# Kernel tuning notes

Measured on AMD Instinct MI355X. Metric: run time of the kernel, lower is better.

## Reference

```python
import jax, jax.numpy as jnp
import numpy as np

B, T, S, D, H, E, K, FF = 4, 1024, 1024, 1024, 16, 8, 2, 4096
DH = D // H
EPS = 1e-5

def layernorm(x, g, b):
    m = x.mean(-1, keepdims=True)
    v = x.var(-1, keepdims=True)
    return (x - m) / jnp.sqrt(v + EPS) * g + b

def mha(q, k, v, mask, wq, bq, wk, bk, wv, bv, wo, bo):
    Bq, Tq, _ = q.shape
    Tk = k.shape[1]
    Q = (q @ wq + bq).reshape(Bq, Tq, H, DH).transpose(0, 2, 1, 3)
    Kh = (k @ wk + bk).reshape(Bq, Tk, H, DH).transpose(0, 2, 1, 3)
    V = (v @ wv + bv).reshape(Bq, Tk, H, DH).transpose(0, 2, 1, 3)
    scores = jnp.einsum('bhqd,bhkd->bhqk', Q, Kh) / (DH ** 0.5)
    scores = jnp.where(mask != 0, scores, jnp.float32(-1e9))
    A = jax.nn.softmax(scores, axis=-1)
    O = jnp.einsum('bhqk,bhkd->bhqd', A, V).transpose(0, 2, 1, 3).reshape(Bq, Tq, D)
    return O @ wo + bo

def sparse_moe(x, wg, bg, w1, b1, w2, b2):
    # x: [B,T,D] -> tokens [N,D]
    Bx, Tx, _ = x.shape
    xt = x.reshape(-1, D)
    N = xt.shape[0]
    probs = jax.nn.softmax(xt @ wg + bg, axis=-1)          # [N,E]
    topv, topi = jax.lax.top_k(probs, K)                    # [N,K]
    topv = topv / topv.sum(-1, keepdims=True)
    gates = jnp.zeros((N, E), xt.dtype).at[jnp.arange(N)[:, None], topi].set(topv)
    h = jax.nn.relu(jnp.einsum('nd,edh->enh', xt, w1) + b1[:, None, :])  # [E,N,FF]
    y = jnp.einsum('enh,ehd->end', h, w2) + b2[:, None, :]               # [E,N,D]
    out = jnp.einsum('ne,end->nd', gates, y)
    return out.reshape(Bx, Tx, D)

def setup_inputs() -> dict:
    key = jax.random.key(0)
    ks = jax.random.split(key, 32)
    r = lambda k, s: jax.random.normal(k, s, dtype=jnp.float32) * 0.02
    inp = {
        'x': jax.random.normal(ks[0], (B, T, D), jnp.float32),
        'encoder_out': jax.random.normal(ks[1], (B, S, D), jnp.float32),
        'src_attn_mask': jnp.ones((B, 1, 1, S), jnp.int32),
        'tgt_attn_mask': jnp.tril(jnp.ones((T, T), jnp.int32))[None, None],
        'ln1_g': jnp.ones((D,), jnp.float32), 'ln1_b': jnp.zeros((D,), jnp.float32),
        'ln2_g': jnp.ones((D,), jnp.float32), 'ln2_b': jnp.zeros((D,), jnp.float32),
        'ln3_g': jnp.ones((D,), jnp.float32), 'ln3_b': jnp.zeros((D,), jnp.float32),
        'wq1': r(ks[2], (D, D)), 'bq1': jnp.zeros((D,), jnp.float32),
        'wk1': r(ks[3], (D, D)), 'bk1': jnp.zeros((D,), jnp.float32),
        'wv1': r(ks[4], (D, D)), 'bv1': jnp.zeros((D,), jnp.float32),
        'wo1': r(ks[5], (D, D)), 'bo1': jnp.zeros((D,), jnp.float32),
        'wq2': r(ks[6], (D, D)), 'bq2': jnp.zeros((D,), jnp.float32),
        'wk2': r(ks[7], (D, D)), 'bk2': jnp.zeros((D,), jnp.float32),
        'wv2': r(ks[8], (D, D)), 'bv2': jnp.zeros((D,), jnp.float32),
        'wo2': r(ks[9], (D, D)), 'bo2': jnp.zeros((D,), jnp.float32),
        'wg': r(ks[10], (D, E)), 'bg': jnp.zeros((E,), jnp.float32),
        'w1': r(ks[11], (E, D, FF)), 'b1': jnp.zeros((E, FF), jnp.float32),
        'w2': r(ks[12], (E, FF, D)), 'b2': jnp.zeros((E, D), jnp.float32),
    }
    return inp

def reference(x, encoder_out, src_attn_mask, tgt_attn_mask,
              ln1_g, ln1_b, ln2_g, ln2_b, ln3_g, ln3_b,
              wq1, bq1, wk1, bk1, wv1, bv1, wo1, bo1,
              wq2, bq2, wk2, bk2, wv2, bv2, wo2, bo2,
              wg, bg, w1, b1, w2, b2):
    # pre-norm residual: x + sublayer(LN(x)); dropout=0 (eval)
    n1 = layernorm(x, ln1_g, ln1_b)
    h1 = x + mha(n1, n1, n1, tgt_attn_mask, wq1, bq1, wk1, bk1, wv1, bv1, wo1, bo1)
    n2 = layernorm(h1, ln2_g, ln2_b)
    h2 = h1 + mha(n2, encoder_out, encoder_out, src_attn_mask, wq2, bq2, wk2, bk2, wv2, bv2, wo2, bo2)
    n3 = layernorm(h2, ln3_g, ln3_b)
    h3 = h2 + sparse_moe(n3, wg, bg, w1, b1, w2, b2)
    return h3
```

## Files before the change

kernel.cpp:

```cpp
#include <hip/hip_runtime.h>

typedef unsigned short u16;
typedef float f32x4 __attribute__((ext_vector_type(4)));
typedef short s16x8 __attribute__((ext_vector_type(8)));
typedef u16   u16x4 __attribute__((ext_vector_type(4)));

#define DEV static __device__ __forceinline__

DEV u16 f2b(float f){
  unsigned u = __builtin_bit_cast(unsigned, f);
  u += 0x7fffu + ((u >> 16) & 1u);
  return (u16)(u >> 16);
}
DEV float b2f(u16 h){ unsigned u = ((unsigned)h) << 16; return __builtin_bit_cast(float, u); }
DEV void tsplit(float v, u16& hv, u16& lv){
  unsigned u = __builtin_bit_cast(unsigned, v);
  hv = (u16)(u >> 16);
  float rest = v - __builtin_bit_cast(float, u & 0xffff0000u);
  lv = (u16)(__builtin_bit_cast(unsigned, rest) >> 16);
}
DEV float fexp2(float x){ float r; asm("v_exp_f32 %0, %1" : "=v"(r) : "v"(x)); return r; }

DEV void glds16(const u16* g, u16* l){
  __builtin_amdgcn_global_load_lds(
      (const __attribute__((address_space(1))) void*)g,
      (__attribute__((address_space(3))) void*)l, 16, 0, 0);
}

DEV f32x4 mfma3(s16x8 ah, s16x8 al, s16x8 bh, s16x8 bl, f32x4 c){
  c = __builtin_amdgcn_mfma_f32_16x16x32_bf16(ah, bh, c, 0, 0, 0);
  c = __builtin_amdgcn_mfma_f32_16x16x32_bf16(ah, bl, c, 0, 0, 0);
  c = __builtin_amdgcn_mfma_f32_16x16x32_bf16(al, bh, c, 0, 0, 0);
  return c;
}

constexpr int TT = 1024, DM = 1024, NE = 8, FFD = 4096;
constexpr int NTOK = 4096;

struct Ptr8 { const float* p[8]; };

__global__ __launch_bounds__(256) void trans8_k(Ptr8 srcs, u16* __restrict__ dh, u16* __restrict__ dl){
  __shared__ float tl[64][65];
  const float* src = srcs.p[blockIdx.z];
  u16* dsth = dh + (size_t)blockIdx.z * 1024 * 1024;
  u16* dstl = dl + (size_t)blockIdx.z * 1024 * 1024;
  const int tid = threadIdx.x;
  const int r0 = blockIdx.y * 64, c0 = blockIdx.x * 64;
  const int ty = tid >> 4, tx = tid & 15;
#pragma unroll
  for (int i = 0; i < 4; i++){
    int row = ty + i * 16;
    f32x4 v = *(const f32x4*)&src[(size_t)(r0 + row) * 1024 + c0 + tx * 4];
#pragma unroll
    for (int j = 0; j < 4; j++) tl[row][tx * 4 + j] = v[j];
  }
  __syncthreads();
#pragma unroll
  for (int i = 0; i < 4; i++){
    int drow = ty + i * 16;
    u16x4 oh, ol;
#pragma unroll
    for (int j = 0; j < 4; j++){
      float v = tl[tx * 4 + j][drow];
      u16 hh, ll; tsplit(v, hh, ll);
      oh[j] = hh; ol[j] = ll;
    }
    *(u16x4*)&dsth[(size_t)(c0 + drow) * 1024 + r0 + tx * 4] = oh;
    *(u16x4*)&dstl[(size_t)(c0 + drow) * 1024 + r0 + tx * 4] = ol;
  }
}

__global__ __launch_bounds__(256) void transb_k(const float* __restrict__ src0, u16* __restrict__ dst0, int R, int C){
  __shared__ float tl[64][65];
  const float* src = src0 + (size_t)blockIdx.z * R * C;
  u16* dst = dst0 + (size_t)blockIdx.z * R * C;
  const int tid = threadIdx.x;
  const int r0 = blockIdx.y * 64, c0 = blockIdx.x * 64;
  const int ty = tid >> 4, tx = tid & 15;
#pragma unroll
  for (int i = 0; i < 4; i++){
    int row = ty + i * 16;
    f32x4 v = *(const f32x4*)&src[(size_t)(r0 + row) * C + c0 + tx * 4];
#pragma unroll
    for (int j = 0; j < 4; j++) tl[row][tx * 4 + j] = v[j];
  }
  __syncthreads();
#pragma unroll
  for (int i = 0; i < 4; i++){
    int drow = ty + i * 16;
    u16x4 o;
#pragma unroll
    for (int j = 0; j < 4; j++) o[j] = f2b(tl[tx * 4 + j][drow]);
    *(u16x4*)&dst[(size_t)(c0 + drow) * R + r0 + tx * 4] = o;
  }
}

__global__ __launch_bounds__(256) void split_k(const float* __restrict__ src,
                                               u16* __restrict__ dh, u16* __restrict__ dl, int n4){
  int i = blockIdx.x * 256 + threadIdx.x;
  if (i < n4){
    f32x4 v = *(const f32x4*)&src[(size_t)i * 4];
    u16x4 oh, ol;
#pragma unroll
    for (int j = 0; j < 4; j++){ u16 hh, ll; tsplit(v[j], hh, ll); oh[j] = hh; ol[j] = ll; }
    *(u16x4*)&dh[(size_t)i * 4] = oh;
    *(u16x4*)&dl[(size_t)i * 4] = ol;
  }
}

__global__ __launch_bounds__(256) void ln_k(const float* __restrict__ x, const float* __restrict__ g,
                                            const float* __restrict__ b,
                                            u16* __restrict__ outH, u16* __restrict__ outL){
  __shared__ float red[8];
  const int row = blockIdx.x, tid = threadIdx.x, l = tid & 63, wave = tid >> 6;
  f32x4 v = *(const f32x4*)&x[(size_t)row * DM + tid * 4];
  float s = v[0] + v[1] + v[2] + v[3];
  float sq = v[0]*v[0] + v[1]*v[1] + v[2]*v[2] + v[3]*v[3];
#pragma unroll
  for (int m = 1; m < 64; m <<= 1){ s += __shfl_xor(s, m); sq += __shfl_xor(sq, m); }
  if (l == 0){ red[wave] = s; red[4 + wave] = sq; }
  __syncthreads();
  float tot = red[0] + red[1] + red[2] + red[3];
  float totq = red[4] + red[5] + red[6] + red[7];
  float mean = tot * (1.0f / DM);
  float var = totq * (1.0f / DM) - mean * mean;
  float rstd = rsqrtf(var + 1e-5f);
  f32x4 gg = *(const f32x4*)&g[tid * 4];
  f32x4 bb = *(const f32x4*)&b[tid * 4];
  u16x4 oh, ol;
#pragma unroll
  for (int j = 0; j < 4; j++){
    float y = (v[j] - mean) * rstd * gg[j] + bb[j];
    u16 hh, ll; tsplit(y, hh, ll); oh[j] = hh; ol[j] = ll;
  }
  *(u16x4*)&outH[(size_t)row * DM + tid * 4] = oh;
  if (outL) *(u16x4*)&outL[(size_t)row * DM + tid * 4] = ol;
}

struct QKVArgs {
  const u16* ah[3]; const u16* al[3]; const float* bias[3];
};

__global__ __launch_bounds__(256) void gemm_qkv3_k(
    QKVArgs args, const u16* __restrict__ Bhp, const u16* __restrict__ Blp,
    u16* __restrict__ QH, u16* __restrict__ QL,
    u16* __restrict__ KH, u16* __restrict__ KL,
    u16* __restrict__ VTH, u16* __restrict__ VTL)
{
  constexpr int K = DM;
  __shared__ alignas(16) u16 LAh[128 * 32], LAl[128 * 32];
  __shared__ alignas(16) u16 LBh[64 * 32], LBl[64 * 32];
  const int tid = threadIdx.x, l = tid & 63, wave = tid >> 6;
  const int seg = blockIdx.z;
  const int m0 = blockIdx.y * 128, n0 = blockIdx.x * 64;
  const int r0 = tid >> 2, seg8 = (tid & 3) * 8;
  const u16* gAh = args.ah[seg] + (size_t)(m0 + r0) * K + seg8;
  const u16* gAl = args.al[seg] + (size_t)(m0 + r0) * K + seg8;
  const u16* gBh = Bhp + (size_t)(seg * 1024 + n0 + r0) * K + seg8;
  const u16* gBl = Blp + (size_t)(seg * 1024 + n0 + r0) * K + seg8;
  u16* wAh = &LAh[wave * 512]; u16* wAl = &LAl[wave * 512];
  u16* wBh = &LBh[wave * 512]; u16* wBl = &LBl[wave * 512];
  const size_t K64 = (size_t)64 * K;
  f32x4 acc[4][2];
#pragma unroll
  for (int i = 0; i < 4; i++)
#pragma unroll
    for (int j = 0; j < 2; j++) acc[i][j] = f32x4{0.f, 0.f, 0.f, 0.f};
  const int wm = (wave >> 1) * 64, wn = (wave & 1) * 32;
  for (int kt = 0; kt < K; kt += 32){
    __syncthreads();
    glds16(gAh + kt, wAh); glds16(gAh + kt + K64, wAh + 2048);
    glds16(gAl + kt, wAl); glds16(gAl + kt + K64, wAl + 2048);
    glds16(gBh + kt, wBh);
    glds16(gBl + kt, wBl);
    __syncthreads();
    s16x8 afh[4], afl[4], bfh[2], bfl[2];
#pragma unroll
    for (int i = 0; i < 4; i++){
      int ar = (wm + i * 16 + (l & 15)) * 32 + (l >> 4) * 8;
      afh[i] = *(const s16x8*)&LAh[ar];
      afl[i] = *(const s16x8*)&LAl[ar];
    }
#pragma unroll
    for (int j = 0; j < 2; j++){
      int br = (wn + j * 16 + (l & 15)) * 32 + (l >> 4) * 8;
      bfh[j] = *(const s16x8*)&LBh[br];
      bfl[j] = *(const s16x8*)&LBl[br];
    }
#pragma unroll
    for (int i = 0; i < 4; i++)
#pragma unroll
      for (int j = 0; j < 2; j++)
        acc[i][j] = mfma3(afh[i], afl[i], bfh[j], bfl[j], acc[i][j]);
  }
  const float* bp = args.bias[seg];
  u16* DH = (seg == 0) ? QH : KH;
  u16* DL = (seg == 0) ? QL : KL;
#pragma unroll
  for (int i = 0; i < 4; i++)
#pragma unroll
    for (int r = 0; r < 4; r++){
      int row = m0 + wm + i * 16 + (l >> 4) * 4 + r;
#pragma unroll
      for (int j = 0; j < 2; j++){
        int col = n0 + wn + j * 16 + (l & 15);
        float v = acc[i][j][r] + bp[col];
        u16 hv, lv; tsplit(v, hv, lv);
        if (seg == 2){
          int bb = row >> 10, tq = row & 1023, hh = col >> 6, dd = col & 63;
          size_t vi = ((size_t)((bb << 4) + hh) * 64 + dd) * 1024 + tq;
          VTH[vi] = hv; VTL[vi] = lv;
        } else {
          size_t idx = (size_t)row * 1024 + col;
          DH[idx] = hv; DL[idx] = lv;
        }
      }
    }
}

__global__ __launch_bounds__(256) void gemm_o64_k(
    const u16* __restrict__ Ahp, const u16* __restrict__ Alp,
    const u16* __restrict__ Bhp, const u16* __restrict__ Blp,
    const float* __restrict__ bias, const float* __restrict__ res,
    float* __restrict__ Cf)
{
  constexpr int K = DM;
  __shared__ alignas(16) u16 LAh[64 * 32], LAl[64 * 32];
  __shared__ alignas(16) u16 LBh[64 * 32], LBl[64 * 32];
  const int tid = threadIdx.x, l = tid & 63, wave = tid >> 6;
  const int m0 = blockIdx.y * 64, n0 = blockIdx.x * 64;
  const int rA = tid >> 2, seg8 = (tid & 3) * 8;
  const u16* gAh = Ahp + (size_t)(m0 + rA) * K + seg8;
  const u16* gAl = Alp + (size_t)(m0 + rA) * K + seg8;
  const u16* gBh = Bhp + (size_t)(n0 + rA) * K + seg8;
  const u16* gBl = Blp + (size_t)(n0 + rA) * K + seg8;
  u16* wAh = &LAh[wave * 512]; u16* wAl = &LAl[wave * 512];
  u16* wBh = &LBh[wave * 512]; u16* wBl = &LBl[wave * 512];
  f32x4 acc[2][2];
#pragma unroll
  for (int i = 0; i < 2; i++)
#pragma unroll
    for (int j = 0; j < 2; j++) acc[i][j] = f32x4{0.f, 0.f, 0.f, 0.f};
  const int wm = (wave >> 1) * 32, wn = (wave & 1) * 32;
  for (int kt = 0; kt < K; kt += 32){
    __syncthreads();
    glds16(gAh + kt, wAh);
    glds16(gAl + kt, wAl);
    glds16(gBh + kt, wBh);
    glds16(gBl + kt, wBl);
    __syncthreads();
    s16x8 afh[2], afl[2], bfh[2], bfl[2];
#pragma unroll
    for (int i = 0; i < 2; i++){
      int ar = (wm + i * 16 + (l & 15)) * 32 + (l >> 4) * 8;
      afh[i] = *(const s16x8*)&LAh[ar];
      afl[i] = *(const s16x8*)&LAl[ar];
    }
#pragma unroll
    for (int j = 0; j < 2; j++){
      int br = (wn + j * 16 + (l & 15)) * 32 + (l >> 4) * 8;
      bfh[j] = *(const s16x8*)&LBh[br];
      bfl[j] = *(const s16x8*)&LBl[br];
    }
#pragma unroll
    for (int i = 0; i < 2; i++)
#pragma unroll
      for (int j = 0; j < 2; j++)
        acc[i][j] = mfma3(afh[i], afl[i], bfh[j], bfl[j], acc[i][j]);
  }
#pragma unroll
  for (int i = 0; i < 2; i++)
#pragma unroll
    for (int r = 0; r < 4; r++){
      int row = m0 + wm + i * 16 + (l >> 4) * 4 + r;
#pragma unroll
      for (int j = 0; j < 2; j++){
        int col = n0 + wn + j * 16 + (l & 15);
        size_t idx = (size_t)row * 1024 + col;
        Cf[idx] = acc[i][j][r] + bias[col] + res[idx];
      }
    }
}

template<bool CAUSAL>
__global__ __launch_bounds__(512) void attn5_k(
    const u16* __restrict__ Qh, const u16* __restrict__ Ql,
    const u16* __restrict__ Kh, const u16* __restrict__ Kl,
    const u16* __restrict__ Vth, const u16* __restrict__ Vtl,
    const int* __restrict__ mask,
    float* __restrict__ OP0, float* __restrict__ OP1,
    float* __restrict__ LS0, float* __restrict__ LS1,
    int Tq, int Tk)
{
  constexpr float CS = 0.125f * 1.4426950408889634f;
  __shared__ alignas(16) u16 KhiL[2048], KloL[2048];
  __shared__ alignas(16) u16 VhiL[2048], VloL[2048];
  __shared__ alignas(16) u16 Plh[8][640], Pll[8][640];
  const int tid = threadIdx.x, l = tid & 63, wave = tid >> 6;
  const int id = blockIdx.x;
  const int bh = ((id >> 3) & 7) * 8 + (id & 7);
  const int b = bh >> 4, h = bh & 15;
  const int qt = (id >> 6) & 7, ks = id >> 9;
  const int q0 = qt * 128;
  float* __restrict__ OP = ks ? OP1 : OP0;
  float* __restrict__ LS = ks ? LS1 : LS0;
  const int ktBeg = ks * 512;
  int lim = CAUSAL ? (q0 + 128) : Tk;
  if (lim > Tk) lim = Tk;
  int ktEnd = (ks + 1) * 512;
  if (ktEnd > lim) ktEnd = lim;

  const int qr = q0 + wave * 16 + (l & 15);
  s16x8 qah[2], qal[2];
#pragma unroll
  for (int kb = 0; kb < 2; kb++){
    size_t base = (size_t)(b * Tq + qr) * DM + h * 64 + kb * 32 + (l >> 4) * 8;
    qah[kb] = *(const s16x8*)(Qh + base);
    qal[kb] = *(const s16x8*)(Ql + base);
  }

  const int sHalf = wave >> 2;
  const int sw = wave & 3;
  const int iS = sw * 64 + l;
  const int keyS = iS >> 3, cKS = iS & 7;
  const u16* gK = (sHalf ? Kl : Kh)
      + (size_t)(b * Tk + ktBeg + keyS) * DM + h * 64 + ((cKS ^ (keyS & 7)) * 8);
  u16* dK = (sHalf ? KloL : KhiL) + sw * 512;
  const int dS = iS >> 2, cVS = iS & 3;
  const size_t vgbase = (size_t)bh * 64 * 1024;
  const u16* gV = (sHalf ? Vtl : Vth)
      + vgbase + (size_t)dS * 1024 + ktBeg + ((cVS ^ ((dS >> 1) & 3)) * 8);
  u16* dV = (sHalf ? VloL : VhiL) + sw * 512;

  float lsum[4] = {0.f, 0.f, 0.f, 0.f};
  f32x4 oacc[4];
#pragma unroll
  for (int nb = 0; nb < 4; nb++) oacc[nb] = f32x4{0.f, 0.f, 0.f, 0.f};
  const int qgr = q0 + wave * 16 + (l >> 4) * 4;

  for (int kt = ktBeg; kt < ktEnd; kt += 32){
    __syncthreads();
    glds16(gK, dK); gK += (size_t)32 * DM;
    glds16(gV, dV); gV += 32;
    __syncthreads();

    f32x4 s[2];
#pragma unroll
    for (int n = 0; n < 2; n++){
      s[n] = f32x4{0.f, 0.f, 0.f, 0.f};
      const int key = n * 16 + (l & 15);
      const int sK = (key & 7);
#pragma unroll
      for (int kb = 0; kb < 2; kb++){
        const int cK = kb * 4 + (l >> 4);
        const int off = key * 64 + ((cK ^ sK) * 8);
        s16x8 kh = *(const s16x8*)&KhiL[off];
        s16x8 klo = *(const s16x8*)&KloL[off];
        s[n] = __builtin_amdgcn_mfma_f32_16x16x32_bf16(qah[kb], kh, s[n], 0, 0, 0);
        s[n] = __builtin_amdgcn_mfma_f32_16x16x32_bf16(qah[kb], klo, s[n], 0, 0, 0);
        s[n] = __builtin_amdgcn_mfma_f32_16x16x32_bf16(qal[kb], kh, s[n], 0, 0, 0);
      }
    }
    int key0 = kt + (l & 15), key1 = key0 + 16;
    int mv0 = 1, mv1 = 1;
    if (!CAUSAL && mask){ mv0 = mask[b * Tk + key0]; mv1 = mask[b * Tk + key1]; }
#pragma unroll
    for (int r = 0; r < 4; r++){
      float p0, p1;
      if (CAUSAL){
        int qg = qgr + r;
        p0 = (key0 <= qg) ? fexp2(s[0][r] * CS) : 0.f;
        p1 = (key1 <= qg) ? fexp2(s[1][r] * CS) : 0.f;
      } else {
        p0 = mv0 ? fexp2(s[0][r] * CS) : 0.f;
        p1 = mv1 ? fexp2(s[1][r] * CS) : 0.f;
      }
      lsum[r] += p0 + p1;
      int po = ((l >> 4) * 4 + r) * 40 + (l & 15);
      u16 h0, l0, h1, l1;
      tsplit(p0, h0, l0); tsplit(p1, h1, l1);
      Plh[wave][po] = h0;      Pll[wave][po] = l0;
      Plh[wave][po + 16] = h1; Pll[wave][po + 16] = l1;
    }
    s16x8 pah = *(const s16x8*)&Plh[wave][(l & 15) * 40 + (l >> 4) * 8];
    s16x8 pal = *(const s16x8*)&Pll[wave][(l & 15) * 40 + (l >> 4) * 8];
#pragma unroll
    for (int nb = 0; nb < 4; nb++){
      const int d = nb * 16 + (l & 15);
      const int off = d * 32 + (((l >> 4) ^ ((d >> 1) & 3)) * 8);
      s16x8 vfh = *(const s16x8*)&VhiL[off];
      s16x8 vfl = *(const s16x8*)&VloL[off];
      oacc[nb] = mfma3(pah, pal, vfh, vfl, oacc[nb]);
    }
  }
#pragma unroll
  for (int r = 0; r < 4; r++){
    float s = lsum[r];
    s += __shfl_xor(s, 1); s += __shfl_xor(s, 2);
    s += __shfl_xor(s, 4); s += __shfl_xor(s, 8);
    int qg = qgr + r;
    if ((l & 15) == 0) LS[(size_t)bh * 1024 + qg] = s;
#pragma unroll
    for (int nb = 0; nb < 4; nb++)
      OP[(size_t)(b * Tq + qg) * DM + h * 64 + nb * 16 + (l & 15)] = oacc[nb][r];
  }
}

__global__ __launch_bounds__(256) void norm_k(
    const float* __restrict__ OP0, const float* __restrict__ OP1,
    const float* __restrict__ LS0, const float* __restrict__ LS1,
    u16* __restrict__ Oh, u16* __restrict__ Ol)
{
  const int t = blockIdx.x, c = threadIdx.x * 4;
  const int b = t >> 10, q = t & 1023, h = c >> 6;
  const size_t li = (size_t)(b * 16 + h) * 1024 + q;
  float inv = 1.0f / (LS0[li] + LS1[li]);
  f32x4 o0 = *(const f32x4*)&OP0[(size_t)t * DM + c];
  f32x4 o1 = *(const f32x4*)&OP1[(size_t)t * DM + c];
  u16x4 oh, ol;
#pragma unroll
  for (int j = 0; j < 4; j++){
    float v = (o0[j] + o1[j]) * inv;
    u16 hh, ll; tsplit(v, hh, ll); oh[j] = hh; ol[j] = ll;
  }
  *(u16x4*)&Oh[(size_t)t * DM + c] = oh;
  *(u16x4*)&Ol[(size_t)t * DM + c] = ol;
}

__global__ __launch_bounds__(256) void moe_gate_k(const float* __restrict__ X,
    const float* __restrict__ g3, const float* __restrict__ b3,
    const float* __restrict__ wg, const float* __restrict__ bg,
    int* __restrict__ cnt, int* __restrict__ perm,
    int* __restrict__ toke, int* __restrict__ tokp, float* __restrict__ tokg)
{
  const int wave = threadIdx.x >> 6, l = threadIdx.x & 63;
  const int t = blockIdx.x * 4 + wave;
  float xv[16];
  float s = 0.f, sq = 0.f;
#pragma unroll
  for (int i = 0; i < 16; i++){
    xv[i] = X[(size_t)t * DM + l + i * 64];
    s += xv[i]; sq += xv[i] * xv[i];
  }
#pragma unroll
  for (int m = 1; m < 64; m <<= 1){ s += __shfl_xor(s, m); sq += __shfl_xor(sq, m); }
  float mean = s * (1.0f / DM);
  float var = sq * (1.0f / DM) - mean * mean;
  float rstd = rsqrtf(var + 1e-5f);
  float acc[8];
#pragma unroll
  for (int e = 0; e < 8; e++) acc[e] = 0.f;
#pragma unroll
  for (int i = 0; i < 16; i++){
    int k = l + i * 64;
    float xn = (xv[i] - mean) * rstd * g3[k] + b3[k];
    f32x4 wa = *(const f32x4*)&wg[k * 8];
    f32x4 wb = *(const f32x4*)&wg[k * 8 + 4];
#pragma unroll
    for (int j = 0; j < 4; j++){ acc[j] += xn * wa[j]; acc[4 + j] += xn * wb[j]; }
  }
#pragma unroll
  for (int e = 0; e < 8; e++)
#pragma unroll
    for (int m = 1; m < 64; m <<= 1) acc[e] += __shfl_xor(acc[e], m);
  if (l == 0){
    float lg[8];
#pragma unroll
    for (int e = 0; e < 8; e++) lg[e] = acc[e] + bg[e];
    float mx = lg[0];
#pragma unroll
    for (int e = 1; e < 8; e++) mx = fmaxf(mx, lg[e]);
    float ex[8]; float sum = 0.f;
#pragma unroll
    for (int e = 0; e < 8; e++){ ex[e] = expf(lg[e] - mx); sum += ex[e]; }
    int i0 = 0;
    for (int e = 1; e < 8; e++) if (ex[e] > ex[i0]) i0 = e;
    int i1 = (i0 == 0) ? 1 : 0;
    for (int e = 0; e < 8; e++) if (e != i0 && ex[e] > ex[i1]) i1 = e;
    float p0 = ex[i0] / sum, p1 = ex[i1] / sum;
    float gs = p0 + p1;
    int pos0 = atomicAdd(&cnt[i0], 1);
    int pos1 = atomicAdd(&cnt[i1], 1);
    perm[i0 * 4096 + pos0] = t;
    perm[i1 * 4096 + pos1] = t;
    toke[2 * t] = i0; toke[2 * t + 1] = i1;
    tokp[2 * t] = pos0; tokp[2 * t + 1] = pos1;
    tokg[2 * t] = p0 / gs; tokg[2 * t + 1] = p1 / gs;
  }
}

__global__ void offsets_k(const int* __restrict__ cnt, int* __restrict__ off){
  if (threadIdx.x == 0){
    int a = 0;
    for (int e = 0; e < 8; e++){ off[e] = a; a += cnt[e]; }
  }
}

__global__ __launch_bounds__(256) void gemm_moe1_k(
    const u16* __restrict__ X, const u16* __restrict__ W1t, const float* __restrict__ b1,
    const int* __restrict__ perm, const int* __restrict__ cnt, const int* __restrict__ off,
    u16* __restrict__ Hb)
{
  const int e = blockIdx.z;
  const int Ce = cnt[e];
  const int mt = blockIdx.y;
  if (mt * 128 >= Ce) return;
  __shared__ alignas(16) u16 Asl[2][128 * 32];
  __shared__ alignas(16) u16 Bsl[2][64 * 32];
  const int tid = threadIdx.x, l = tid & 63, wave = tid >> 6;
  const int n0 = blockIdx.x * 64;
  const int r0 = tid >> 2, seg = (tid & 3) * 8;
  const int rl0 = mt * 128 + r0, rl1 = rl0 + 64;
  const int g0 = perm[e * 4096 + (rl0 < Ce ? rl0 : Ce - 1)];
  const int g1 = perm[e * 4096 + (rl1 < Ce ? rl1 : Ce - 1)];
  const u16* gA0 = X + (size_t)g0 * DM + seg;
  const u16* gA1 = X + (size_t)g1 * DM + seg;
  const u16* gB = W1t + (size_t)e * FFD * DM + (size_t)(n0 + r0) * DM + seg;
  u16* wA0 = &Asl[0][wave * 512]; u16* wA1 = &Asl[1][wave * 512];
  u16* wB0 = &Bsl[0][wave * 512]; u16* wB1 = &Bsl[1][wave * 512];
  f32x4 acc[4][2];
#pragma unroll
  for (int i = 0; i < 4; i++)
#pragma unroll
    for (int j = 0; j < 2; j++) acc[i][j] = f32x4{0.f,0.f,0.f,0.f};
  const int wm = (wave >> 1) * 64, wn = (wave & 1) * 32;
  for (int kt = 0; kt < DM; kt += 64){
    __syncthreads();
    glds16(gA0 + kt, wA0);      glds16(gA1 + kt, wA0 + 2048);
    glds16(gA0 + kt + 32, wA1); glds16(gA1 + kt + 32, wA1 + 2048);
    glds16(gB + kt, wB0);
    glds16(gB + kt + 32, wB1);
    __syncthreads();
#pragma unroll
    for (int p = 0; p < 2; p++){
      s16x8 af[4], bfr[2];
#pragma unroll
      for (int i = 0; i < 4; i++)
        af[i]  = *(const s16x8*)&Asl[p][(wm + i * 16 + (l & 15)) * 32 + (l >> 4) * 8];
#pragma unroll
      for (int j = 0; j < 2; j++)
        bfr[j] = *(const s16x8*)&Bsl[p][(wn + j * 16 + (l & 15)) * 32 + (l >> 4) * 8];
#pragma unroll
      for (int i = 0; i < 4; i++)
#pragma unroll
        for (int j = 0; j < 2; j++)
          acc[i][j] = __builtin_amdgcn_mfma_f32_16x16x32_bf16(af[i], bfr[j], acc[i][j], 0, 0, 0);
    }
  }
  const int base = off[e];
#pragma unroll
  for (int i = 0; i < 4; i++)
#pragma unroll
    for (int r = 0; r < 4; r++){
      int rloc = mt * 128 + wm + i * 16 + (l >> 4) * 4 + r;
      if (rloc < Ce){
#pragma unroll
        for (int j = 0; j < 2; j++){
          int col = n0 + wn + j * 16 + (l & 15);
          float v = acc[i][j][r] + b1[e * FFD + col];
          v = fmaxf(v, 0.f);
          Hb[(size_t)(base + rloc) * FFD + col] = f2b(v);
        }
      }
    }
}

__global__ __launch_bounds__(256) void gemm_moe2_k(
    const u16* __restrict__ Hb, const u16* __restrict__ W2t,
    const int* __restrict__ cnt, const int* __restrict__ off,
    u16* __restrict__ YP0, u16* __restrict__ YP1)
{
  const int z = blockIdx.z;
  const int e = z & 7, ks = z >> 3;
  const int Ce = cnt[e];
  const int mt = blockIdx.y;
  if (mt * 128 >= Ce) return;
  u16* __restrict__ Y = ks ? YP1 : YP0;
  __shared__ alignas(16) u16 Asl[2][128 * 32];
  __shared__ alignas(16) u16 Bsl[2][64 * 32];
  const int tid = threadIdx.x, l = tid & 63, wave = tid >> 6;
  const int n0 = blockIdx.x * 64;
  const int r0 = tid >> 2, seg = (tid & 3) * 8;
  const int base = off[e];
  const int rl0 = mt * 128 + r0, rl1 = rl0 + 64;
  const int a0r = base + (rl0 < Ce ? rl0 : Ce - 1);
  const int a1r = base + (rl1 < Ce ? rl1 : Ce - 1);
  const u16* gA0 = Hb + (size_t)a0r * FFD + seg;
  const u16* gA1 = Hb + (size_t)a1r * FFD + seg;
  const u16* gB = W2t + (size_t)e * DM * FFD + (size_t)(n0 + r0) * FFD + seg;
  u16* wA0 = &Asl[0][wave * 512]; u16* wA1 = &Asl[1][wave * 512];
  u16* wB0 = &Bsl[0][wave * 512]; u16* wB1 = &Bsl[1][wave * 512];
  f32x4 acc[4][2];
#pragma unroll
  for (int i = 0; i < 4; i++)
#pragma unroll
    for (int j = 0; j < 2; j++) acc[i][j] = f32x4{0.f,0.f,0.f,0.f};
  const int wm = (wave >> 1) * 64, wn = (wave & 1) * 32;
  const int kBeg = ks * (FFD / 2), kEnd = kBeg + FFD / 2;
  for (int kt = kBeg; kt < kEnd; kt += 64){
    __syncthreads();
    glds16(gA0 + kt, wA0);      glds16(gA1 + kt, wA0 + 2048);
    glds16(gA0 + kt + 32, wA1); glds16(gA1 + kt + 32, wA1 + 2048);
    glds16(gB + kt, wB0);
    glds16(gB + kt + 32, wB1);
    __syncthreads();
#pragma unroll
    for (int p = 0; p < 2; p++){
      s16x8 af[4], bfr[2];
#pragma unroll
      for (int i = 0; i < 4; i++)
        af[i]  = *(const s16x8*)&Asl[p][(wm + i * 16 + (l & 15)) * 32 + (l >> 4) * 8];
#pragma unroll
      for (int j = 0; j < 2; j++)
        bfr[j] = *(const s16x8*)&Bsl[p][(wn + j * 16 + (l & 15)) * 32 + (l >> 4) * 8];
#pragma unroll
      for (int i = 0; i < 4; i++)
#pragma unroll
        for (int j = 0; j < 2; j++)
          acc[i][j] = __builtin_amdgcn_mfma_f32_16x16x32_bf16(af[i], bfr[j], acc[i][j], 0, 0, 0);
    }
  }
#pragma unroll
  for (int i = 0; i < 4; i++)
#pragma unroll
    for (int r = 0; r < 4; r++){
      int rloc = mt * 128 + wm + i * 16 + (l >> 4) * 4 + r;
      if (rloc < Ce){
#pragma unroll
        for (int j = 0; j < 2; j++){
          int col = n0 + wn + j * 16 + (l & 15);
          Y[(size_t)(base + rloc) * DM + col] = f2b(acc[i][j][r]);
        }
      }
    }
}

__global__ __launch_bounds__(256) void combine_k(const float* __restrict__ h2,
    const u16* __restrict__ YP0, const u16* __restrict__ YP1,
    const int* __restrict__ toke, const int* __restrict__ tokp, const float* __restrict__ tokg,
    const int* __restrict__ off, const float* __restrict__ b2, float* __restrict__ out)
{
  const int t = blockIdx.x;
  const int c = threadIdx.x * 4;
  int e0 = toke[2 * t], e1 = toke[2 * t + 1];
  size_t r0 = (size_t)off[e0] + tokp[2 * t];
  size_t r1 = (size_t)off[e1] + tokp[2 * t + 1];
  float g0 = tokg[2 * t], g1 = tokg[2 * t + 1];
  f32x4 a  = *(const f32x4*)&h2[(size_t)t * DM + c];
  u16x4 ya0 = *(const u16x4*)&YP0[r0 * DM + c];
  u16x4 ya1 = *(const u16x4*)&YP1[r0 * DM + c];
  u16x4 yb0 = *(const u16x4*)&YP0[r1 * DM + c];
  u16x4 yb1 = *(const u16x4*)&YP1[r1 * DM + c];
  f32x4 v0 = *(const f32x4*)&b2[(size_t)e0 * DM + c];
  f32x4 v1 = *(const f32x4*)&b2[(size_t)e1 * DM + c];
  f32x4 o;
#pragma unroll
  for (int j = 0; j < 4; j++){
    float yA = b2f(ya0[j]) + b2f(ya1[j]);
    float yB = b2f(yb0[j]) + b2f(yb1[j]);
    o[j] = a[j] + (yA + v0[j]) * g0 + (yB + v1[j]) * g1;
  }
  *(f32x4*)&out[(size_t)t * DM + c] = o;
}

extern "C" void kernel_launch(void* const* d_in, const int* in_sizes, int n_in,
                              void* d_out, int out_size, void* d_ws, size_t ws_size,
                              hipStream_t stream) {
  const float* x    = (const float*)d_in[0];
  const float* enc  = (const float*)d_in[1];
  const int* smask  = (const int*)d_in[2];
  const float* ln1g = (const float*)d_in[4]; const float* ln1b = (const float*)d_in[5];
  const float* ln2g = (const float*)d_in[6]; const float* ln2b = (const float*)d_in[7];
  const float* ln3g = (const float*)d_in[8]; const float* ln3b = (const float*)d_in[9];
  const float* wq1 = (const float*)d_in[10]; const float* bq1 = (const float*)d_in[11];
  const float* wk1 = (const float*)d_in[12]; const float* bk1 = (const float*)d_in[13];
  const float* wv1 = (const float*)d_in[14]; const float* bv1 = (const float*)d_in[15];
  const float* wo1 = (const float*)d_in[16]; const float* bo1 = (const float*)d_in[17];
  const float* wq2 = (const float*)d_in[18]; const float* bq2 = (const float*)d_in[19];
  const float* wk2 = (const float*)d_in[20]; const float* bk2 = (const float*)d_in[21];
  const float* wv2 = (const float*)d_in[22]; const float* bv2 = (const float*)d_in[23];
  const float* wo2 = (const float*)d_in[24]; const float* bo2 = (const float*)d_in[25];
  const float* wg  = (const float*)d_in[26]; const float* bg  = (const float*)d_in[27];
  const float* w1  = (const float*)d_in[28]; const float* b1  = (const float*)d_in[29];
  const float* w2  = (const float*)d_in[30]; const float* b2  = (const float*)d_in[31];

  const size_t MB = 1024ull * 1024ull;
  char* ws = (char*)d_ws;
  size_t o = 0;
  auto alloc = [&](size_t bytes) -> void* {
    void* p = ws + o;
    o += (bytes + 255) & ~(size_t)255;
    return p;
  };
  float* H1  = (float*)alloc(16 * MB);
  float* H2  = (float*)alloc(16 * MB);
  u16*  NBF  = (u16*) alloc(8 * MB);
  int* CNT  = (int*)alloc(256);
  int* OFF  = (int*)alloc(256);
  int* PERM = (int*)alloc((size_t)8 * 4096 * 4);
  int* TOKE = (int*)alloc((size_t)NTOK * 2 * 4);
  int* TOKP = (int*)alloc((size_t)NTOK * 2 * 4);
  float* TOKG = (float*)alloc((size_t)NTOK * 2 * 4);
  char* R = (char*)alloc(224 * MB);
  u16* WTH = (u16*)(R);
  u16* WTL = (u16*)(R + 16 * MB);
  u16* NH  = (u16*)(R + 32 * MB);
  u16* NL  = (u16*)(R + 40 * MB);
  u16* EH  = (u16*)(R + 48 * MB);
  u16* EL  = (u16*)(R + 56 * MB);
  u16* QH  = (u16*)(R + 64 * MB);
  u16* QL  = (u16*)(R + 72 * MB);
  u16* KH  = (u16*)(R + 80 * MB);
  u16* KL  = (u16*)(R + 88 * MB);
  u16* VTH = (u16*)(R + 96 * MB);
  u16* VTL = (u16*)(R + 104 * MB);
  u16* OH  = (u16*)(R + 112 * MB);
  u16* OL  = (u16*)(R + 120 * MB);
  float* OP0 = (float*)(R + 128 * MB);
  float* OP1 = (float*)(R + 144 * MB);
  float* LS0 = (float*)(R + 160 * MB);
  float* LS1 = (float*)(R + 161 * MB);
  u16* W1T = (u16*)(R);
  u16* W2T = (u16*)(R + 64 * MB);
  u16* HB  = (u16*)(R + 128 * MB);
  u16* YP0 = (u16*)(R + 192 * MB);
  u16* YP1 = (u16*)(R + 208 * MB);

  Ptr8 p8; p8.p[0]=wq1; p8.p[1]=wk1; p8.p[2]=wv1; p8.p[3]=wo1;
           p8.p[4]=wq2; p8.p[5]=wk2; p8.p[6]=wv2; p8.p[7]=wo2;
  trans8_k<<<dim3(16,16,8), 256, 0, stream>>>(p8, WTH, WTL);
  split_k<<<dim3(4096), 256, 0, stream>>>(enc, EH, EL, NTOK * DM / 4);

  const size_t W = (size_t)1024 * 1024;
  ln_k<<<dim3(NTOK), 256, 0, stream>>>(x, ln1g, ln1b, NH, NL);
  {
    QKVArgs a;
    a.ah[0]=NH; a.ah[1]=NH; a.ah[2]=NH;
    a.al[0]=NL; a.al[1]=NL; a.al[2]=NL;
    a.bias[0]=bq1; a.bias[1]=bk1; a.bias[2]=bv1;
    gemm_qkv3_k<<<dim3(16,32,3), 256, 0, stream>>>(a, WTH + 0*W, WTL + 0*W,
                                                   QH, QL, KH, KL, VTH, VTL);
  }
  attn5_k<true><<<dim3(1024), 512, 0, stream>>>(QH, QL, KH, KL, VTH, VTL, nullptr,
                                                OP0, OP1, LS0, LS1, TT, TT);
  norm_k<<<dim3(NTOK), 256, 0, stream>>>(OP0, OP1, LS0, LS1, OH, OL);
  gemm_o64_k<<<dim3(16,64), 256, 0, stream>>>(OH, OL, WTH + 3*W, WTL + 3*W, bo1, x, H1);

  ln_k<<<dim3(NTOK), 256, 0, stream>>>(H1, ln2g, ln2b, NH, NL);
  {
    QKVArgs a;
    a.ah[0]=NH; a.ah[1]=EH; a.ah[2]=EH;
    a.al[0]=NL; a.al[1]=EL; a.al[2]=EL;
    a.bias[0]=bq2; a.bias[1]=bk2; a.bias[2]=bv2;
    gemm_qkv3_k<<<dim3(16,32,3), 256, 0, stream>>>(a, WTH + 4*W, WTL + 4*W,
                                                   QH, QL, KH, KL, VTH, VTL);
  }
  attn5_k<false><<<dim3(1024), 512, 0, stream>>>(QH, QL, KH, KL, VTH, VTL, smask,
                                                 OP0, OP1, LS0, LS1, TT, TT);
  norm_k<<<dim3(NTOK), 256, 0, stream>>>(OP0, OP1, LS0, LS1, OH, OL);
  gemm_o64_k<<<dim3(16,64), 256, 0, stream>>>(OH, OL, WTH + 7*W, WTL + 7*W, bo2, H1, H2);

  transb_k<<<dim3(64,16,8), 256, 0, stream>>>(w1, W1T, 1024, 4096);
  transb_k<<<dim3(16,64,8), 256, 0, stream>>>(w2, W2T, 4096, 1024);
  ln_k<<<dim3(NTOK), 256, 0, stream>>>(H2, ln3g, ln3b, NBF, nullptr);
  hipMemsetAsync(CNT, 0, 8 * sizeof(int), stream);
  moe_gate_k<<<dim3(1024), 256, 0, stream>>>(H2, ln3g, ln3b, wg, bg, CNT, PERM, TOKE, TOKP, TOKG);
  offsets_k<<<dim3(1), 64, 0, stream>>>(CNT, OFF);
  gemm_moe1_k<<<dim3(64,32,8), 256, 0, stream>>>(NBF, W1T, b1, PERM, CNT, OFF, HB);
  gemm_moe2_k<<<dim3(16,32,16), 256, 0, stream>>>(HB, W2T, CNT, OFF, YP0, YP1);
  combine_k<<<dim3(NTOK), 256, 0, stream>>>(H2, YP0, YP1, TOKE, TOKP, TOKG, OFF, b2, (float*)d_out);
}
```

Baseline: 900.2 us.

## Enlarge MoE down-projection tile to 128x128, drop split-K, emit fp32 output

The second expert GEMM now uses 512-thread blocks computing 128x128 output tiles over the full FF dimension, instead of 128x64 tiles split in two along K. Blocks are indexed through a flattened 1D grid with the expert in the low bits. The result is written once in fp32, and the combine kernel reads a single fp32 buffer instead of summing two bf16 partials. The aim is more operand reuse per loaded tile and no partial-sum traffic. In exchange there are fewer and longer blocks, which may worsen load balance and tail effects, and fp32 stores double the bytes per output element.

```diff
diff --git a/kernel.cpp b/kernel.cpp
--- a/kernel.cpp
+++ b/kernel.cpp
@@ -565,28 +565,25 @@
     }
 }
 
-__global__ __launch_bounds__(256) void gemm_moe2_k(
+__global__ __launch_bounds__(512) void gemm_moe2_k(
     const u16* __restrict__ Hb, const u16* __restrict__ W2t,
-    const int* __restrict__ cnt, const int* __restrict__ off,
-    u16* __restrict__ YP0, u16* __restrict__ YP1)
+    const int* __restrict__ cnt, const int* __restrict__ off, float* __restrict__ Y)
 {
-  const int z = blockIdx.z;
-  const int e = z & 7, ks = z >> 3;
+  const int id = blockIdx.x;
+  const int e = id & 7;
+  const int rest = id >> 3;
+  const int n0 = (rest & 7) * 128;
+  const int mt = rest >> 3;
   const int Ce = cnt[e];
-  const int mt = blockIdx.y;
   if (mt * 128 >= Ce) return;
-  u16* __restrict__ Y = ks ? YP1 : YP0;
   __shared__ alignas(16) u16 Asl[2][128 * 32];
-  __shared__ alignas(16) u16 Bsl[2][64 * 32];
+  __shared__ alignas(16) u16 Bsl[2][128 * 32];
   const int tid = threadIdx.x, l = tid & 63, wave = tid >> 6;
-  const int n0 = blockIdx.x * 64;
   const int r0 = tid >> 2, seg = (tid & 3) * 8;
   const int base = off[e];
-  const int rl0 = mt * 128 + r0, rl1 = rl0 + 64;
-  const int a0r = base + (rl0 < Ce ? rl0 : Ce - 1);
-  const int a1r = base + (rl1 < Ce ? rl1 : Ce - 1);
-  const u16* gA0 = Hb + (size_t)a0r * FFD + seg;
-  const u16* gA1 = Hb + (size_t)a1r * FFD + seg;
+  const int rl = mt * 128 + r0;
+  const int ar = base + (rl < Ce ? rl : Ce - 1);
+  const u16* gA = Hb + (size_t)ar * FFD + seg;
   const u16* gB = W2t + (size_t)e * DM * FFD + (size_t)(n0 + r0) * FFD + seg;
   u16* wA0 = &Asl[0][wave * 512]; u16* wA1 = &Asl[1][wave * 512];
   u16* wB0 = &Bsl[0][wave * 512]; u16* wB1 = &Bsl[1][wave * 512];
@@ -595,12 +592,11 @@
   for (int i = 0; i < 4; i++)
 #pragma unroll
     for (int j = 0; j < 2; j++) acc[i][j] = f32x4{0.f,0.f,0.f,0.f};
-  const int wm = (wave >> 1) * 64, wn = (wave & 1) * 32;
-  const int kBeg = ks * (FFD / 2), kEnd = kBeg + FFD / 2;
-  for (int kt = kBeg; kt < kEnd; kt += 64){
-    __syncthreads();
-    glds16(gA0 + kt, wA0);      glds16(gA1 + kt, wA0 + 2048);
-    glds16(gA0 + kt + 32, wA1); glds16(gA1 + kt + 32, wA1 + 2048);
+  const int wm = (wave >> 2) * 64, wn = (wave & 3) * 32;
+  for (int kt = 0; kt < FFD; kt += 64){
+    __syncthreads();
+    glds16(gA + kt, wA0);
+    glds16(gA + kt + 32, wA1);
     glds16(gB + kt, wB0);
     glds16(gB + kt + 32, wB1);
     __syncthreads();
@@ -629,14 +625,14 @@
 #pragma unroll
         for (int j = 0; j < 2; j++){
           int col = n0 + wn + j * 16 + (l & 15);
-          Y[(size_t)(base + rloc) * DM + col] = f2b(acc[i][j][r]);
+          Y[(size_t)(base + rloc) * DM + col] = acc[i][j][r];
         }
       }
     }
 }
 
 __global__ __launch_bounds__(256) void combine_k(const float* __restrict__ h2,
-    const u16* __restrict__ YP0, const u16* __restrict__ YP1,
+    const float* __restrict__ Y,
     const int* __restrict__ toke, const int* __restrict__ tokp, const float* __restrict__ tokg,
     const int* __restrict__ off, const float* __restrict__ b2, float* __restrict__ out)
 {
@@ -647,19 +643,11 @@
   size_t r1 = (size_t)off[e1] + tokp[2 * t + 1];
   float g0 = tokg[2 * t], g1 = tokg[2 * t + 1];
   f32x4 a  = *(const f32x4*)&h2[(size_t)t * DM + c];
-  u16x4 ya0 = *(const u16x4*)&YP0[r0 * DM + c];
-  u16x4 ya1 = *(const u16x4*)&YP1[r0 * DM + c];
-  u16x4 yb0 = *(const u16x4*)&YP0[r1 * DM + c];
-  u16x4 yb1 = *(const u16x4*)&YP1[r1 * DM + c];
+  f32x4 y0 = *(const f32x4*)&Y[r0 * DM + c];
+  f32x4 y1 = *(const f32x4*)&Y[r1 * DM + c];
   f32x4 v0 = *(const f32x4*)&b2[(size_t)e0 * DM + c];
   f32x4 v1 = *(const f32x4*)&b2[(size_t)e1 * DM + c];
-  f32x4 o;
-#pragma unroll
-  for (int j = 0; j < 4; j++){
-    float yA = b2f(ya0[j]) + b2f(ya1[j]);
-    float yB = b2f(yb0[j]) + b2f(yb1[j]);
-    o[j] = a[j] + (yA + v0[j]) * g0 + (yB + v1[j]) * g1;
-  }
+  f32x4 o = a + (y0 + v0) * g0 + (y1 + v1) * g1;
   *(f32x4*)&out[(size_t)t * DM + c] = o;
 }
 
@@ -723,8 +711,7 @@
   u16* W1T = (u16*)(R);
   u16* W2T = (u16*)(R + 64 * MB);
   u16* HB  = (u16*)(R + 128 * MB);
-  u16* YP0 = (u16*)(R + 192 * MB);
-  u16* YP1 = (u16*)(R + 208 * MB);
+  float* YB = (float*)(R + 192 * MB);
 
   Ptr8 p8; p8.p[0]=wq1; p8.p[1]=wk1; p8.p[2]=wv1; p8.p[3]=wo1;
            p8.p[4]=wq2; p8.p[5]=wk2; p8.p[6]=wv2; p8.p[7]=wo2;
@@ -767,6 +754,6 @@
   moe_gate_k<<<dim3(1024), 256, 0, stream>>>(H2, ln3g, ln3b, wg, bg, CNT, PERM, TOKE, TOKP, TOKG);
   offsets_k<<<dim3(1), 64, 0, stream>>>(CNT, OFF);
   gemm_moe1_k<<<dim3(64,32,8), 256, 0, stream>>>(NBF, W1T, b1, PERM, CNT, OFF, HB);
-  gemm_moe2_k<<<dim3(16,32,16), 256, 0, stream>>>(HB, W2T, CNT, OFF, YP0, YP1);
-  combine_k<<<dim3(NTOK), 256, 0, stream>>>(H2, YP0, YP1, TOKE, TOKP, TOKG, OFF, b2, (float*)d_out);
-}
+  gemm_moe2_k<<<dim3(2048), 512, 0, stream>>>(HB, W2T, CNT, OFF, YB);
+  combine_k<<<dim3(NTOK), 256, 0, stream>>>(H2, YB, TOKE, TOKP, TOKG, OFF, b2, (float*)d_out);
+}
```

After: 848.4 us. 5.8% less time.
